# Kernel optimization log

Measured on AMD Instinct MI355X. Metric: run time of the kernel, lower is better.

Reference implementation:

```python
import jax, jax.numpy as jnp
import numpy as np

B, IN_DIM, HIDDEN, N_CLASSES, D_Z = 16384, 1024, 2048, 8, 256
LN_EPS = 1e-5  # torch.nn.LayerNorm default


def _l2_normalize(x, axis=1, eps=1e-12):
    # matches F.normalize: x / max(||x||, eps)
    n = jnp.sqrt(jnp.sum(x * x, axis=axis, keepdims=True))
    return x / jnp.maximum(n, eps)


def setup_inputs() -> dict:
    key = jax.random.key(0)
    ks = jax.random.split(key, 9)
    s1 = 1.0 / np.sqrt(IN_DIM)
    s2 = 1.0 / np.sqrt(HIDDEN)
    return {
        "feat": jax.random.normal(ks[0], (B, IN_DIM), dtype=jnp.float32),
        "z_cat": jax.random.normal(ks[1], (B, D_Z), dtype=jnp.float32),
        "mu_cat": jax.random.normal(ks[2], (N_CLASSES, D_Z), dtype=jnp.float32),
        "ln_gamma": jnp.ones((N_CLASSES, IN_DIM), dtype=jnp.float32),
        "ln_beta": jnp.zeros((N_CLASSES, IN_DIM), dtype=jnp.float32),
        "W1": jax.random.uniform(ks[3], (N_CLASSES, IN_DIM, HIDDEN), jnp.float32, -s1, s1),
        "b1": jax.random.uniform(ks[4], (N_CLASSES, HIDDEN), jnp.float32, -s1, s1),
        "W2": jax.random.uniform(ks[5], (N_CLASSES, HIDDEN, N_CLASSES), jnp.float32, -s2, s2),
        "b2": jax.random.uniform(ks[6], (N_CLASSES, N_CLASSES), jnp.float32, -s2, s2),
        "tau_gate": 1,
    }


def reference(feat, z_cat, mu_cat, ln_gamma, ln_beta, W1, b1, W2, b2, tau_gate):
    # --- cosine-similarity softmax gate ---
    zn = _l2_normalize(z_cat, axis=1)            # [B, Dz]
    mun = _l2_normalize(mu_cat, axis=1)          # [E, Dz]
    sims = zn @ mun.T                            # [B, E]
    tau = max(1e-6, float(tau_gate))
    w = jax.nn.softmax(sims / tau, axis=1)       # [B, E]

    # --- batched experts: LN -> Linear -> ReLU -> (Dropout=identity, eval) -> Linear ---
    mu = jnp.mean(feat, axis=-1, keepdims=True)
    var = jnp.mean(jnp.square(feat - mu), axis=-1, keepdims=True)
    xhat = (feat - mu) * jax.lax.rsqrt(var + LN_EPS)            # [B, D] (shared)
    x_e = xhat[None] * ln_gamma[:, None, :] + ln_beta[:, None, :]  # [E, B, D]
    h = jax.nn.relu(jnp.einsum('ebd,edh->ebh', x_e, W1) + b1[:, None, :])  # [E, B, H]
    exp_logits = jnp.einsum('ebh,ehc->ebc', h, W2) + b2[:, None, :]        # [E, B, C]

    # --- gate-weighted sum over experts ---
    logits = jnp.einsum('ebc,be->bc', exp_logits, w)  # [B, C]
    return logits, w
```

## Files before the change

### kernel.cpp

```cpp
#include <hip/hip_runtime.h>
#include <hip/hip_bf16.h>
#include <cstdint>

#define NB     16384
#define DIN    1024
#define HID    2048
#define NE     8
#define NC     8
#define DZ     256

#define BM     256
#define BNB    128
#define BK     64
#define KSTEPS (DIN/BK)
#define NUNITS 2048
#define GRID_MAIN 512

typedef short bf16x8 __attribute__((ext_vector_type(8)));
typedef float f32x4  __attribute__((ext_vector_type(4)));

__device__ __forceinline__ unsigned short f2bf(float f) {
    unsigned int u = __float_as_uint(f);
    unsigned int r = (u + 0x7FFFu + ((u >> 16) & 1u)) >> 16;
    return (unsigned short)r;
}

__device__ __forceinline__ void async_copy16(const void* g, void* l) {
    __builtin_amdgcn_global_load_lds(
        (const __attribute__((address_space(1))) unsigned int*)g,
        (__attribute__((address_space(3))) unsigned int*)l, 16, 0, 0);
}

__global__ __launch_bounds__(256) void k_gate(const float* __restrict__ z,
                                              const float* __restrict__ mu,
                                              const int* __restrict__ tau_i,
                                              const float* __restrict__ b2,
                                              float* __restrict__ wout,
                                              float* __restrict__ logits) {
    int row = blockIdx.x * 4 + (threadIdx.x >> 6);
    int l = threadIdx.x & 63;
    float4 zv = *(const float4*)&z[(size_t)row * DZ + l * 4];
    float zz = zv.x * zv.x + zv.y * zv.y + zv.z * zv.z + zv.w * zv.w;
    float dots[NE], mm[NE];
#pragma unroll
    for (int e = 0; e < NE; ++e) {
        float4 m = *(const float4*)&mu[e * DZ + l * 4];
        dots[e] = zv.x * m.x + zv.y * m.y + zv.z * m.z + zv.w * m.w;
        mm[e]   = m.x * m.x + m.y * m.y + m.z * m.z + m.w * m.w;
    }
#pragma unroll
    for (int off = 32; off; off >>= 1) {
        zz += __shfl_xor(zz, off);
#pragma unroll
        for (int e = 0; e < NE; ++e) {
            dots[e] += __shfl_xor(dots[e], off);
            mm[e]   += __shfl_xor(mm[e], off);
        }
    }
    float zn = fmaxf(sqrtf(zz), 1e-12f);
    float tau = fmaxf(1e-6f, (float)tau_i[0]);
    float s[NE], mx = -1e30f;
#pragma unroll
    for (int e = 0; e < NE; ++e) {
        s[e] = dots[e] / (zn * fmaxf(sqrtf(mm[e]), 1e-12f)) / tau;
        mx = fmaxf(mx, s[e]);
    }
    float sum = 0.f;
#pragma unroll
    for (int e = 0; e < NE; ++e) { s[e] = expf(s[e] - mx); sum += s[e]; }
    float inv = 1.f / sum;
    if (l < NE) {
        wout[(size_t)row * NE + l] = s[l] * inv;
        float acc = 0.f;
#pragma unroll
        for (int e = 0; e < NE; ++e) acc += s[e] * inv * b2[e * NC + l];
        logits[(size_t)row * NC + l] = acc;
    }
}

__global__ __launch_bounds__(256) void k_ln(const float* __restrict__ feat,
                                            unsigned short* __restrict__ xhat) {
    int row = blockIdx.x;
    int t = threadIdx.x;
    float4 v = *(const float4*)&feat[(size_t)row * DIN + t * 4];
    float s  = v.x + v.y + v.z + v.w;
    float sq = v.x * v.x + v.y * v.y + v.z * v.z + v.w * v.w;
#pragma unroll
    for (int off = 32; off; off >>= 1) {
        s  += __shfl_down(s, off);
        sq += __shfl_down(sq, off);
    }
    __shared__ float ls[8];
    int w = t >> 6, l = t & 63;
    if (l == 0) { ls[w] = s; ls[4 + w] = sq; }
    __syncthreads();
    s  = ls[0] + ls[1] + ls[2] + ls[3];
    sq = ls[4] + ls[5] + ls[6] + ls[7];
    float mean = s * (1.f / DIN);
    float var  = sq * (1.f / DIN) - mean * mean;
    float r = 1.0f / sqrtf(var + 1e-5f);
    uint2 p;
    p.x = (unsigned)f2bf((v.x - mean) * r) | ((unsigned)f2bf((v.y - mean) * r) << 16);
    p.y = (unsigned)f2bf((v.z - mean) * r) | ((unsigned)f2bf((v.w - mean) * r) << 16);
    *(uint2*)&xhat[(size_t)row * DIN + t * 4] = p;
}

__global__ __launch_bounds__(256) void k_w2prep(const float* __restrict__ W2,
                                                const float* __restrict__ b1,
                                                unsigned short* __restrict__ w2t,
                                                float* __restrict__ b1p,
                                                int* __restrict__ qcounter) {
    int i = blockIdx.x * 256 + threadIdx.x;
    if (i == 0) qcounter[0] = 0;
    int e = i >> 15;
    int rem = i & 32767;
    int c = rem >> 11;
    int h = rem & 2047;
    float v = (c < NC) ? W2[((size_t)(e * HID + h)) * NC + c] : 0.f;
    w2t[i] = f2bf(v);
    if (i < NE * HID) b1p[i] = b1[i];
}

__global__ __launch_bounds__(256) void k_w1prep(const float* __restrict__ W1,
                                                const float* __restrict__ gamma,
                                                const float* __restrict__ beta,
                                                unsigned short* __restrict__ w1t,
                                                float* __restrict__ b1p) {
    __shared__ float tile[64][65];
    int e  = blockIdx.z;
    int d0 = blockIdx.y * 64;
    int h0 = blockIdx.x * 64;
    int tx = threadIdx.x & 15, ty = threadIdx.x >> 4;
#pragma unroll
    for (int rr = 0; rr < 4; ++rr) {
        int d = ty + rr * 16;
        float4 v = *(const float4*)&W1[((size_t)e * DIN + d0 + d) * HID + h0 + tx * 4];
        tile[tx * 4 + 0][d] = v.x;
        tile[tx * 4 + 1][d] = v.y;
        tile[tx * 4 + 2][d] = v.z;
        tile[tx * 4 + 3][d] = v.w;
    }
    __syncthreads();
    float4 g = *(const float4*)&gamma[(size_t)e * DIN + d0 + tx * 4];
#pragma unroll
    for (int rr = 0; rr < 4; ++rr) {
        int h = ty + rr * 16;
        uint2 p;
        p.x = (unsigned)f2bf(tile[h][tx * 4 + 0] * g.x) |
              ((unsigned)f2bf(tile[h][tx * 4 + 1] * g.y) << 16);
        p.y = (unsigned)f2bf(tile[h][tx * 4 + 2] * g.z) |
              ((unsigned)f2bf(tile[h][tx * 4 + 3] * g.w) << 16);
        *(uint2*)&w1t[((size_t)e * HID + h0 + h) * DIN + d0 + tx * 4] = p;
    }
    if (threadIdx.x < 64) {
        int h = threadIdx.x;
        float sacc = 0.f;
        for (int r = 0; r < 64; ++r)
            sacc += beta[(size_t)e * DIN + d0 + r] * tile[h][r];
        atomicAdd(&b1p[(size_t)e * HID + h0 + h], sacc);
    }
}

__global__ __launch_bounds__(256, 2) void moe_main(
        const unsigned short* __restrict__ xhat,
        const unsigned short* __restrict__ w1t,
        const float* __restrict__ b1p,
        const unsigned short* __restrict__ w2t,
        const float* __restrict__ wg,
        float* __restrict__ logits,
        int* __restrict__ qcounter) {
    __shared__ __align__(16) short lds_a[BM * BK];
    __shared__ __align__(16) short lds_b[BNB * BK];
    __shared__ __align__(16) char  lds_ht[4 * 64 * 80];
    __shared__ int s_u;

    const int t = threadIdx.x;
    const int w = t >> 6, l = t & 63;
    const int q = l >> 4, ml = l & 15;
    const int wm = (w >> 1) * 128;
    const int wn = (w & 1) * 64;

    const int strow  = w * 8 + (l >> 3);
    const int kslot8 = (((l & 7) ^ ((l >> 3) & 7))) * 8;
    const int rswz   = ml & 7;
    char* myht = lds_ht + w * 5120;

    for (;;) {
        if (t == 0) s_u = atomicAdd(qcounter, 1);
        __syncthreads();
        const int u = s_u;
        if (u >= NUNITS) break;
        const int btile = u & 127;
        const int e     = (u >> 7) & 7;
        const int half  = u >> 10;
        const int b0 = btile * BNB;
        const unsigned short* gA = w1t + (size_t)e * HID * DIN;
        const unsigned short* gB = xhat + (size_t)b0 * DIN;

        f32x4 acc2[4];
#pragma unroll
        for (int tb = 0; tb < 4; ++tb) acc2[tb] = (f32x4){0.f, 0.f, 0.f, 0.f};

        for (int ch = half * 4; ch < half * 4 + 4; ++ch) {
            const int hid0 = ch * BM;
            f32x4 acc[8][4];
#pragma unroll
            for (int i = 0; i < 8; ++i)
#pragma unroll
                for (int j = 0; j < 4; ++j) acc[i][j] = (f32x4){0.f, 0.f, 0.f, 0.f};

            for (int ks = 0; ks < KSTEPS; ++ks) {
                const int k0 = ks * BK;
#pragma unroll
                for (int it = 0; it < 8; ++it) {
                    const int row = it * 32 + strow;
                    async_copy16(gA + (size_t)(hid0 + row) * DIN + k0 + kslot8,
                                 (char*)lds_a + it * 4096 + w * 1024 + (l << 4));
                    if (it < 4)
                        async_copy16(gB + (size_t)row * DIN + k0 + kslot8,
                                     (char*)lds_b + it * 4096 + w * 1024 + (l << 4));
                }
                __syncthreads();
#pragma unroll 1
                for (int kk = 0; kk < 2; ++kk) {
                    const int cswz = ((kk * 4 + q) ^ rswz) * 8;
                    bf16x8 bF[4];
#pragma unroll
                    for (int j = 0; j < 4; ++j)
                        bF[j] = *(const bf16x8*)&lds_b[(wn + 16 * j + ml) * BK + cswz];
#pragma unroll
                    for (int i = 0; i < 8; ++i) {
                        const bf16x8 aF =
                            *(const bf16x8*)&lds_a[(wm + 16 * i + ml) * BK + cswz];
#pragma unroll
                        for (int j = 0; j < 4; ++j)
                            acc[i][j] = __builtin_amdgcn_mfma_f32_16x16x32_bf16(
                                aF, bF[j], acc[i][j], 0, 0, 0);
                    }
                }
                __syncthreads();
            }

#pragma unroll
            for (int s = 0; s < 4; ++s) {
#pragma unroll
                for (int i2 = 0; i2 < 2; ++i2) {
                    const int i = 2 * s + i2;
                    const float4 bias = *(const float4*)
                        &b1p[(size_t)e * HID + hid0 + wm + 16 * i + 4 * q];
#pragma unroll
                    for (int j = 0; j < 4; ++j) {
                        float v0 = fmaxf(acc[i][j].x + bias.x, 0.f);
                        float v1 = fmaxf(acc[i][j].y + bias.y, 0.f);
                        float v2 = fmaxf(acc[i][j].z + bias.z, 0.f);
                        float v3 = fmaxf(acc[i][j].w + bias.w, 0.f);
                        uint2 p;
                        p.x = (unsigned)f2bf(v0) | ((unsigned)f2bf(v1) << 16);
                        p.y = (unsigned)f2bf(v2) | ((unsigned)f2bf(v3) << 16);
                        const int brow = 16 * j + ml;
                        *(uint2*)(myht + brow * 80 + (16 * i2 + 4 * q) * 2) = p;
                    }
                }
                const bf16x8 b2f = *(const bf16x8*)&w2t[((size_t)e * 16 + ml) * HID +
                                                        hid0 + wm + 32 * s + 8 * q];
#pragma unroll
                for (int tb = 0; tb < 4; ++tb) {
                    const bf16x8 a2f =
                        *(const bf16x8*)(myht + (16 * tb + ml) * 80 + q * 16);
                    acc2[tb] = __builtin_amdgcn_mfma_f32_16x16x32_bf16(
                        a2f, b2f, acc2[tb], 0, 0, 0);
                }
            }
        }

        __syncthreads();
        float* red = (float*)lds_ht;
        if (w >= 2) {
            float* dst = red + ((size_t)((w & 1) * 64 + l)) * 16;
#pragma unroll
            for (int tb = 0; tb < 4; ++tb)
#pragma unroll
                for (int r = 0; r < 4; ++r) dst[tb * 4 + r] = acc2[tb][r];
        }
        __syncthreads();
        if (w < 2) {
            const float* src = red + ((size_t)((w & 1) * 64 + l)) * 16;
            const int c = ml;
            if (c < NC) {
#pragma unroll
                for (int tb = 0; tb < 4; ++tb) {
#pragma unroll
                    for (int r = 0; r < 4; ++r) {
                        float v = acc2[tb][r] + src[tb * 4 + r];
                        const int bg = b0 + wn + 16 * tb + 4 * q + r;
                        const float wgt = wg[(size_t)bg * NE + e];
                        atomicAdd(&logits[(size_t)bg * NC + c], wgt * v);
                    }
                }
            }
        }
    }
}

extern "C" void kernel_launch(void* const* d_in, const int* in_sizes, int n_in,
                              void* d_out, int out_size, void* d_ws, size_t ws_size,
                              hipStream_t stream) {
    const float* feat  = (const float*)d_in[0];
    const float* z     = (const float*)d_in[1];
    const float* mu    = (const float*)d_in[2];
    const float* gamma = (const float*)d_in[3];
    const float* beta  = (const float*)d_in[4];
    const float* W1    = (const float*)d_in[5];
    const float* b1    = (const float*)d_in[6];
    const float* W2    = (const float*)d_in[7];
    const float* b2    = (const float*)d_in[8];
    const int*   tau   = (const int*)d_in[9];

    float* logits = (float*)d_out;
    float* wout   = logits + (size_t)NB * NC;

    char* ws = (char*)d_ws;
    unsigned short* xhat = (unsigned short*)ws;
    unsigned short* w1t  = (unsigned short*)(ws + 33554432);
    unsigned short* w2t  = (unsigned short*)(ws + 67108864);
    float*          b1p  = (float*)(ws + 67633152);
    int*            qcnt = (int*)(ws + 67698688);

    k_gate<<<NB / 4, 256, 0, stream>>>(z, mu, tau, b2, wout, logits);
    k_ln<<<NB, 256, 0, stream>>>(feat, xhat);
    k_w2prep<<<(NE * 16 * HID) / 256, 256, 0, stream>>>(W2, b1, w2t, b1p, qcnt);
    k_w1prep<<<dim3(HID / 64, DIN / 64, NE), 256, 0, stream>>>(W1, gamma, beta, w1t, b1p);
    moe_main<<<dim3(GRID_MAIN), 256, 0, stream>>>(xhat, w1t, b1p, w2t,
                                                  wout, logits, qcnt);
}
```

Baseline: 724.7 us.

## Restructure MoE GEMM into 512-thread blocks with a four-stage async LDS pipeline

Replaces the atomic work-queue and the two-barrier-per-k-step 256-thread GEMM with statically assigned 512-thread blocks. Each block owns one expert and two 256-row batch tiles and walks all hidden chunks. The K loop now uses BK=32 tiles in a four-buffer ring of async global-to-LDS copies, with explicit vmcnt waits so loads run three tiles ahead, plus s_setprio around the MFMA bursts. This is meant to hide global load latency and raise MFMA utilisation, at the cost of 128KB of LDS per block, which likely limits occupancy to one block per CU. It also loses the dynamic load balancing of the work queue.

```diff
diff --git a/kernel.cpp b/kernel.cpp
--- a/kernel.cpp
+++ b/kernel.cpp
@@ -9,12 +9,9 @@
 #define NC     8
 #define DZ     256
 
-#define BM     256
-#define BNB    128
-#define BK     64
-#define KSTEPS (DIN/BK)
-#define NUNITS 2048
-#define GRID_MAIN 512
+#define BK2    32
+#define NKT    (DIN / BK2)
+#define GRID_MAIN 256
 
 typedef short bf16x8 __attribute__((ext_vector_type(8)));
 typedef float f32x4  __attribute__((ext_vector_type(4)));
@@ -108,10 +105,8 @@
 __global__ __launch_bounds__(256) void k_w2prep(const float* __restrict__ W2,
                                                 const float* __restrict__ b1,
                                                 unsigned short* __restrict__ w2t,
-                                                float* __restrict__ b1p,
-                                                int* __restrict__ qcounter) {
+                                                float* __restrict__ b1p) {
     int i = blockIdx.x * 256 + threadIdx.x;
-    if (i == 0) qcounter[0] = 0;
     int e = i >> 15;
     int rem = i & 32767;
     int c = rem >> 11;
@@ -161,85 +156,89 @@
     }
 }
 
-__global__ __launch_bounds__(256, 2) void moe_main(
+
+#define WAITV(n_) asm volatile("s_waitcnt vmcnt(" #n_ ")" ::: "memory")
+#define BAR()  do { __builtin_amdgcn_s_barrier(); __builtin_amdgcn_sched_barrier(0); } while (0)
+
+#define STAGE(tile_) do {                                                     \
+    char* dst_ = (char*)lds + (((tile_) & 3) << 15) + (t << 4);               \
+    const size_t ro_ = (size_t)srow * DIN + (size_t)(tile_) * BK2 + sk;       \
+    async_copy16(gA + ro_, dst_);                                             \
+    async_copy16(gA + ro_ + (size_t)128 * DIN, dst_ + 8192);                  \
+    async_copy16(gB + ro_, dst_ + 16384);                                     \
+    async_copy16(gB + ro_ + (size_t)128 * DIN, dst_ + 24576);                 \
+} while (0)
+
+#define KBODY(kt_) do {                                                       \
+    const short* la_ = (const short*)(lds + (((kt_) & 3) << 15));             \
+    const short* lb_ = la_ + 8192;                                            \
+    bf16x8 bF_[4];                                                            \
+    _Pragma("unroll")                                                         \
+    for (int j_ = 0; j_ < 4; ++j_)                                            \
+        bF_[j_] = *(const bf16x8*)&lb_[(wn + 16 * j_ + ml) * BK2 + cswz];     \
+    __builtin_amdgcn_s_setprio(1);                                            \
+    _Pragma("unroll")                                                         \
+    for (int i_ = 0; i_ < 8; ++i_) {                                          \
+        const bf16x8 aF_ = *(const bf16x8*)&la_[(wm + 16 * i_ + ml) * BK2 + cswz]; \
+        _Pragma("unroll")                                                     \
+        for (int j_ = 0; j_ < 4; ++j_)                                        \
+            acc[i_][j_] = __builtin_amdgcn_mfma_f32_16x16x32_bf16(            \
+                aF_, bF_[j_], acc[i_][j_], 0, 0, 0);                          \
+    }                                                                         \
+    __builtin_amdgcn_s_setprio(0);                                            \
+} while (0)
+
+__global__ __launch_bounds__(512, 2) void moe_main(
         const unsigned short* __restrict__ xhat,
         const unsigned short* __restrict__ w1t,
         const float* __restrict__ b1p,
         const unsigned short* __restrict__ w2t,
         const float* __restrict__ wg,
-        float* __restrict__ logits,
-        int* __restrict__ qcounter) {
-    __shared__ __align__(16) short lds_a[BM * BK];
-    __shared__ __align__(16) short lds_b[BNB * BK];
-    __shared__ __align__(16) char  lds_ht[4 * 64 * 80];
-    __shared__ int s_u;
-
-    const int t = threadIdx.x;
-    const int w = t >> 6, l = t & 63;
-    const int q = l >> 4, ml = l & 15;
-    const int wm = (w >> 1) * 128;
-    const int wn = (w & 1) * 64;
-
-    const int strow  = w * 8 + (l >> 3);
-    const int kslot8 = (((l & 7) ^ ((l >> 3) & 7))) * 8;
-    const int rswz   = ml & 7;
-    char* myht = lds_ht + w * 5120;
-
-    for (;;) {
-        if (t == 0) s_u = atomicAdd(qcounter, 1);
-        __syncthreads();
-        const int u = s_u;
-        if (u >= NUNITS) break;
-        const int btile = u & 127;
-        const int e     = (u >> 7) & 7;
-        const int half  = u >> 10;
-        const int b0 = btile * BNB;
-        const unsigned short* gA = w1t + (size_t)e * HID * DIN;
+        float* __restrict__ logits) {
+    __shared__ __align__(16) char lds[131072];
+
+    const int t  = threadIdx.x;
+    const int w  = t >> 6, l = t & 63;
+    const int q  = l >> 4, ml = l & 15;
+    const int wm = (w >> 2) * 128;
+    const int wn = (w & 3) * 64;
+    const int cswz = (q ^ (ml & 3)) * 8;
+    const int srow = t >> 2;
+    const int sk   = ((t & 3) ^ (srow & 3)) * 8;
+
+    const int e    = blockIdx.x & 7;
+    const int slot = blockIdx.x >> 3;
+    char* myht = (char*)lds + w * 5120;
+
+    for (int pr = 0; pr < 2; ++pr) {
+        const int b0 = (pr * 32 + slot) * 256;
         const unsigned short* gB = xhat + (size_t)b0 * DIN;
 
         f32x4 acc2[4];
 #pragma unroll
         for (int tb = 0; tb < 4; ++tb) acc2[tb] = (f32x4){0.f, 0.f, 0.f, 0.f};
 
-        for (int ch = half * 4; ch < half * 4 + 4; ++ch) {
-            const int hid0 = ch * BM;
+        for (int ms = 0; ms < 8; ++ms) {
+            const int hid0 = ms * 256;
+            const unsigned short* gA = w1t + ((size_t)e * HID + hid0) * DIN;
+
             f32x4 acc[8][4];
 #pragma unroll
             for (int i = 0; i < 8; ++i)
 #pragma unroll
                 for (int j = 0; j < 4; ++j) acc[i][j] = (f32x4){0.f, 0.f, 0.f, 0.f};
 
-            for (int ks = 0; ks < KSTEPS; ++ks) {
-                const int k0 = ks * BK;
-#pragma unroll
-                for (int it = 0; it < 8; ++it) {
-                    const int row = it * 32 + strow;
-                    async_copy16(gA + (size_t)(hid0 + row) * DIN + k0 + kslot8,
-                                 (char*)lds_a + it * 4096 + w * 1024 + (l << 4));
-                    if (it < 4)
-                        async_copy16(gB + (size_t)row * DIN + k0 + kslot8,
-                                     (char*)lds_b + it * 4096 + w * 1024 + (l << 4));
-                }
-                __syncthreads();
+            STAGE(0); STAGE(1); STAGE(2);
 #pragma unroll 1
-                for (int kk = 0; kk < 2; ++kk) {
-                    const int cswz = ((kk * 4 + q) ^ rswz) * 8;
-                    bf16x8 bF[4];
-#pragma unroll
-                    for (int j = 0; j < 4; ++j)
-                        bF[j] = *(const bf16x8*)&lds_b[(wn + 16 * j + ml) * BK + cswz];
-#pragma unroll
-                    for (int i = 0; i < 8; ++i) {
-                        const bf16x8 aF =
-                            *(const bf16x8*)&lds_a[(wm + 16 * i + ml) * BK + cswz];
-#pragma unroll
-                        for (int j = 0; j < 4; ++j)
-                            acc[i][j] = __builtin_amdgcn_mfma_f32_16x16x32_bf16(
-                                aF, bF[j], acc[i][j], 0, 0, 0);
-                    }
-                }
-                __syncthreads();
+            for (int kt = 0; kt < NKT - 3; ++kt) {
+                WAITV(8);
+                BAR();
+                STAGE(kt + 3);
+                KBODY(kt);
             }
+            WAITV(8); BAR(); KBODY(29);
+            WAITV(4); BAR(); KBODY(30);
+            WAITV(0); BAR(); KBODY(31);
 
 #pragma unroll
             for (int s = 0; s < 4; ++s) {
@@ -257,8 +256,7 @@
                         uint2 p;
                         p.x = (unsigned)f2bf(v0) | ((unsigned)f2bf(v1) << 16);
                         p.y = (unsigned)f2bf(v2) | ((unsigned)f2bf(v3) << 16);
-                        const int brow = 16 * j + ml;
-                        *(uint2*)(myht + brow * 80 + (16 * i2 + 4 * q) * 2) = p;
+                        *(uint2*)(myht + (16 * j + ml) * 80 + (16 * i2 + 4 * q) * 2) = p;
                     }
                 }
                 const bf16x8 b2f = *(const bf16x8*)&w2t[((size_t)e * 16 + ml) * HID +
@@ -271,34 +269,34 @@
                         a2f, b2f, acc2[tb], 0, 0, 0);
                 }
             }
+            __syncthreads();
         }
 
-        __syncthreads();
-        float* red = (float*)lds_ht;
-        if (w >= 2) {
-            float* dst = red + ((size_t)((w & 1) * 64 + l)) * 16;
+        float* red = (float*)(lds + 65536);
+        if (w >= 4) {
+            float* dst = red + ((w & 3) * 64 + l) * 16;
 #pragma unroll
             for (int tb = 0; tb < 4; ++tb)
 #pragma unroll
                 for (int r = 0; r < 4; ++r) dst[tb * 4 + r] = acc2[tb][r];
         }
         __syncthreads();
-        if (w < 2) {
-            const float* src = red + ((size_t)((w & 1) * 64 + l)) * 16;
-            const int c = ml;
-            if (c < NC) {
+        if (w < 4) {
+            const float* src = red + (w * 64 + l) * 16;
+            if (ml < NC) {
 #pragma unroll
                 for (int tb = 0; tb < 4; ++tb) {
 #pragma unroll
                     for (int r = 0; r < 4; ++r) {
                         float v = acc2[tb][r] + src[tb * 4 + r];
                         const int bg = b0 + wn + 16 * tb + 4 * q + r;
-                        const float wgt = wg[(size_t)bg * NE + e];
-                        atomicAdd(&logits[(size_t)bg * NC + c], wgt * v);
+                        atomicAdd(&logits[(size_t)bg * NC + ml],
+                                  wg[(size_t)bg * NE + e] * v);
                     }
                 }
             }
         }
+        __syncthreads();
     }
 }
 
@@ -324,12 +322,10 @@
     unsigned short* w1t  = (unsigned short*)(ws + 33554432);
     unsigned short* w2t  = (unsigned short*)(ws + 67108864);
     float*          b1p  = (float*)(ws + 67633152);
-    int*            qcnt = (int*)(ws + 67698688);
 
     k_gate<<<NB / 4, 256, 0, stream>>>(z, mu, tau, b2, wout, logits);
     k_ln<<<NB, 256, 0, stream>>>(feat, xhat);
-    k_w2prep<<<(NE * 16 * HID) / 256, 256, 0, stream>>>(W2, b1, w2t, b1p, qcnt);
+    k_w2prep<<<(NE * 16 * HID) / 256, 256, 0, stream>>>(W2, b1, w2t, b1p);
     k_w1prep<<<dim3(HID / 64, DIN / 64, NE), 256, 0, stream>>>(W1, gamma, beta, w1t, b1p);
-    moe_main<<<dim3(GRID_MAIN), 256, 0, stream>>>(xhat, w1t, b1p, w2t,
-                                                  wout, logits, qcnt);
-}
+    moe_main<<<dim3(GRID_MAIN), 512, 0, stream>>>(xhat, w1t, b1p, w2t, wout, logits);
+}
```

New measurement: 703.4 us. 1.03x faster.
